# Kernel optimization log

Measured on AMD Instinct MI355X. Metric: run time of the kernel, lower is better.

Reference implementation:

```python
import jax, jax.numpy as jnp
import numpy as np
import math

B, S, D, H, DQ, DV, DI, L, V = 8, 512, 1024, 16, 64, 64, 4096, 6, 32000
EPS = 1e-5


def sinusoidal_pe(s, d):
    pos = np.arange(s)[:, None].astype(np.float64)
    i = np.arange(d)[None, :]
    angle = pos / np.power(10000.0, (2 * (i // 2)) / d)
    pe = np.where(i % 2 == 0, np.sin(angle), np.cos(angle))
    return jnp.asarray(pe, dtype=jnp.float32)  # [S, D]


def setup_inputs() -> dict:
    key = jax.random.key(0)
    ks = jax.random.split(key, 12)
    std = 0.02
    return {
        "tokens": jax.random.randint(ks[0], (B, S), 0, V),
        "lengths": jax.random.randint(ks[1], (B,), S // 2 + 1, S + 1),
        "emb": jax.random.normal(ks[2], (V, D), jnp.float32) * std,
        "Wq": jax.random.normal(ks[3], (L, D, H * DQ), jnp.float32) * std,
        "bq": jnp.zeros((L, H * DQ), jnp.float32),
        "Wkv": jax.random.normal(ks[4], (L, D, H * (DQ + DV)), jnp.float32) * std,
        "bkv": jnp.zeros((L, H * (DQ + DV)), jnp.float32),
        "Wo": jax.random.normal(ks[5], (L, H * DV, D), jnp.float32) * std,
        "bo": jnp.zeros((L, D), jnp.float32),
        "ln_attn_g": jnp.ones((L, D), jnp.float32),
        "ln_attn_b": jnp.zeros((L, D), jnp.float32),
        "W1": jax.random.normal(ks[6], (L, D, DI), jnp.float32) * std,
        "b1": jnp.zeros((L, DI), jnp.float32),
        "W2": jax.random.normal(ks[7], (L, DI, D), jnp.float32) * std,
        "b2": jnp.zeros((L, D), jnp.float32),
        "ln_ffn_g": jnp.ones((L, D), jnp.float32),
        "ln_ffn_b": jnp.zeros((L, D), jnp.float32),
        "ln_f_g": jnp.ones((D,), jnp.float32),
        "ln_f_b": jnp.zeros((D,), jnp.float32),
    }


def layer_norm(x, g, b):
    m = jnp.mean(x, axis=-1, keepdims=True)
    v = jnp.var(x, axis=-1, keepdims=True)
    return (x - m) / jnp.sqrt(v + EPS) * g + b


def encoder_forward(tokens, lengths, emb, Wq, bq, Wkv, bkv, Wo, bo,
                    ln_attn_g, ln_attn_b, W1, b1, W2, b2,
                    ln_ffn_g, ln_ffn_b, ln_f_g, ln_f_b):
    x = emb[tokens] * math.sqrt(D) + sinusoidal_pe(S, D)[None]  # [B,S,D]
    key_mask = jnp.arange(S)[None, :] < lengths[:, None]        # [B,S] valid keys
    scale = 1.0 / math.sqrt(DQ)

    def layer(x, p):
        wq, bq_, wkv, bkv_, wo, bo_, g1, be1, w1, bf1, w2, bf2, g2, be2 = p
        # --- multi-head self-attention sublayer (pre-LN, residual from raw x) ---
        h = layer_norm(x, g1, be1)
        q = (h @ wq + bq_).reshape(B, S, H, DQ)
        kv = h @ wkv + bkv_
        k = kv[..., : H * DQ].reshape(B, S, H, DQ)
        v = kv[..., H * DQ:].reshape(B, S, H, DV)
        scores = jnp.einsum('bqhd,bkhd->bhqk', q, k) * scale
        scores = jnp.where(key_mask[:, None, None, :], scores, -jnp.inf)
        a = jax.nn.softmax(scores, axis=-1)
        o = jnp.einsum('bhqk,bkhd->bqhd', a, v).reshape(B, S, H * DV)
        x = x + o @ wo + bo_
        # --- position-wise FFN sublayer (pre-LN, residual) ---
        h2 = layer_norm(x, g2, be2)
        x = x + jax.nn.relu(h2 @ w1 + bf1) @ w2 + bf2
        return x, None

    x, _ = jax.lax.scan(layer, x, (Wq, bq, Wkv, bkv, Wo, bo,
                                   ln_attn_g, ln_attn_b, W1, b1, W2, b2,
                                   ln_ffn_g, ln_ffn_b))
    return layer_norm(x, ln_f_g, ln_f_b)


def reference(tokens, lengths, emb, Wq, bq, Wkv, bkv, Wo, bo,
              ln_attn_g, ln_attn_b, W1, b1, W2, b2,
              ln_ffn_g, ln_ffn_b, ln_f_g, ln_f_b):
    return encoder_forward(tokens, lengths, emb, Wq, bq, Wkv, bkv, Wo, bo,
                           ln_attn_g, ln_attn_b, W1, b1, W2, b2,
                           ln_ffn_g, ln_ffn_b, ln_f_g, ln_f_b)
```

## Files before the change

kernel.cpp:

```cpp
#include <hip/hip_runtime.h>
#include <hip/hip_bf16.h>
#include <math.h>

typedef __bf16 bf16;
typedef bf16 bf16x8 __attribute__((ext_vector_type(8)));
typedef bf16 bf16x4v __attribute__((ext_vector_type(4)));
typedef float f32x4 __attribute__((ext_vector_type(4)));

typedef const __attribute__((address_space(1))) void* gp_t;
typedef __attribute__((address_space(3))) void* lp_t;

#define SB 512
#define DM 1024

__global__ __launch_bounds__(256) void embed_kernel(
    const int* __restrict__ tokens, const float* __restrict__ emb,
    float* __restrict__ x)
{
  const int row = blockIdx.x;
  const int s = row & (SB - 1);
  const int tok = tokens[row];
  const int c = threadIdx.x * 4;
  const float4 e = *(const float4*)&emb[(size_t)tok * DM + c];
  const float ev[4] = {e.x, e.y, e.z, e.w};
  float o[4];
#pragma unroll
  for (int u = 0; u < 4; ++u) {
    int i = c + u;
    int j = i & ~1;
    float freq = __expf(-9.210340371976184f * (float)j * (1.0f / (float)DM));
    float ang = (float)s * freq;
    float pe = ((i & 1) == 0) ? __sinf(ang) : __cosf(ang);
    o[u] = ev[u] * 32.0f + pe;
  }
  *(float4*)&x[(size_t)row * DM + c] = make_float4(o[0], o[1], o[2], o[3]);
}

template<bool OUTBF>
__global__ __launch_bounds__(256) void ln_kernel(
    const float* __restrict__ x, const float* __restrict__ g,
    const float* __restrict__ b, bf16* __restrict__ outB,
    float* __restrict__ outF)
{
  __shared__ float red[8];
  const int row = blockIdx.x, tid = threadIdx.x;
  const float4 v = *(const float4*)&x[(size_t)row * DM + tid * 4];
  float s = v.x + v.y + v.z + v.w;
  float sq = v.x * v.x + v.y * v.y + v.z * v.z + v.w * v.w;
#pragma unroll
  for (int off = 32; off > 0; off >>= 1) {
    s  += __shfl_xor(s, off);
    sq += __shfl_xor(sq, off);
  }
  if ((tid & 63) == 0) { red[tid >> 6] = s; red[4 + (tid >> 6)] = sq; }
  __syncthreads();
  const float ts = red[0] + red[1] + red[2] + red[3];
  const float tq = red[4] + red[5] + red[6] + red[7];
  const float mean = ts * (1.0f / DM);
  const float var  = tq * (1.0f / DM) - mean * mean;
  const float rstd = rsqrtf(var + 1e-5f);
  const int c = tid * 4;
  const float4 gv = *(const float4*)&g[c];
  const float4 bv = *(const float4*)&b[c];
  const float o0 = (v.x - mean) * rstd * gv.x + bv.x;
  const float o1 = (v.y - mean) * rstd * gv.y + bv.y;
  const float o2 = (v.z - mean) * rstd * gv.z + bv.z;
  const float o3 = (v.w - mean) * rstd * gv.w + bv.w;
  if constexpr (OUTBF) {
    bf16x4v ov = {(bf16)o0, (bf16)o1, (bf16)o2, (bf16)o3};
    *(bf16x4v*)&outB[(size_t)row * DM + c] = ov;
  } else {
    *(float4*)&outF[(size_t)row * DM + c] = make_float4(o0, o1, o2, o3);
  }
}

template<int NS, bool OUTBF, bool WRITEX>
__global__ __launch_bounds__(256) void red_ln_kernel(
    const float* __restrict__ x, const float* __restrict__ part,
    const float* __restrict__ badd, const float* __restrict__ g,
    const float* __restrict__ b, float* __restrict__ xout,
    bf16* __restrict__ outB, float* __restrict__ outF)
{
  __shared__ float red[8];
  const int row = blockIdx.x, tid = threadIdx.x;
  const int c = tid * 4;
  const size_t base = (size_t)row * DM + c;
  float4 v = *(const float4*)&x[base];
  const float4 ba = *(const float4*)&badd[c];
  v.x += ba.x; v.y += ba.y; v.z += ba.z; v.w += ba.w;
#pragma unroll
  for (int z = 0; z < NS; ++z) {
    const float4 pv = *(const float4*)&part[(size_t)z * 4096 * DM + base];
    v.x += pv.x; v.y += pv.y; v.z += pv.z; v.w += pv.w;
  }
  if constexpr (WRITEX) *(float4*)&xout[base] = v;
  float s = v.x + v.y + v.z + v.w;
  float sq = v.x * v.x + v.y * v.y + v.z * v.z + v.w * v.w;
#pragma unroll
  for (int off = 32; off > 0; off >>= 1) {
    s  += __shfl_xor(s, off);
    sq += __shfl_xor(sq, off);
  }
  if ((tid & 63) == 0) { red[tid >> 6] = s; red[4 + (tid >> 6)] = sq; }
  __syncthreads();
  const float ts = red[0] + red[1] + red[2] + red[3];
  const float tq = red[4] + red[5] + red[6] + red[7];
  const float mean = ts * (1.0f / DM);
  const float var  = tq * (1.0f / DM) - mean * mean;
  const float rstd = rsqrtf(var + 1e-5f);
  const float4 gv = *(const float4*)&g[c];
  const float4 bv = *(const float4*)&b[c];
  const float o0 = (v.x - mean) * rstd * gv.x + bv.x;
  const float o1 = (v.y - mean) * rstd * gv.y + bv.y;
  const float o2 = (v.z - mean) * rstd * gv.z + bv.z;
  const float o3 = (v.w - mean) * rstd * gv.w + bv.w;
  if constexpr (OUTBF) {
    bf16x4v ov = {(bf16)o0, (bf16)o1, (bf16)o2, (bf16)o3};
    *(bf16x4v*)&outB[(size_t)row * DM + c] = ov;
  } else {
    *(float4*)&outF[(size_t)row * DM + c] = make_float4(o0, o1, o2, o3);
  }
}

__global__ __launch_bounds__(256) void wtrans_kernel(
    const float* __restrict__ W, bf16* __restrict__ Wt, int N, int K)
{
  __shared__ __attribute__((aligned(16))) bf16 T[64][72];
  const int tid = threadIdx.x;
  const int n0 = blockIdx.x * 64;
  const int k0 = blockIdx.y * 64;
#pragma unroll
  for (int p = 0; p < 4; ++p) {
    const int flat = p * 1024 + tid * 4;
    const int kr = flat >> 6;
    const int nc = flat & 63;
    const float4 v = *(const float4*)&W[(size_t)(k0 + kr) * N + n0 + nc];
    T[nc + 0][kr] = (bf16)v.x;
    T[nc + 1][kr] = (bf16)v.y;
    T[nc + 2][kr] = (bf16)v.z;
    T[nc + 3][kr] = (bf16)v.w;
  }
  __syncthreads();
#pragma unroll
  for (int p = 0; p < 2; ++p) {
    const int flat = p * 2048 + tid * 8;
    const int nr = flat >> 6;
    const int kc = flat & 63;
    const bf16x8 v = *(const bf16x8*)&T[nr][kc];
    *(bf16x8*)&Wt[(size_t)(n0 + nr) * K + k0 + kc] = v;
  }
}

__global__ __launch_bounds__(256) void bias_concat_kernel(
    const float* __restrict__ bq, const float* __restrict__ bkv,
    float* __restrict__ bqkv)
{
  const int i = blockIdx.x * 256 + threadIdx.x;
  const int l = i / 3072, j = i - l * 3072;
  bqkv[i] = (j < 1024) ? bq[l * 1024 + j] : bkv[l * 2048 + (j - 1024)];
}

template<bool RELU, bool RESID, bool OUTBF, bool SPLITK>
__global__ __launch_bounds__(256) void gemm128(
    const bf16* __restrict__ A, const bf16* __restrict__ Bt,
    const float* __restrict__ bias, const float* __restrict__ resid,
    bf16* __restrict__ outB, float* __restrict__ outF,
    int M, int N, int K)
{
  __shared__ __attribute__((aligned(16))) bf16 As[128][32];
  __shared__ __attribute__((aligned(16))) bf16 Bs[128][32];
  const int tid  = threadIdx.x;
  const int lane = tid & 63;
  const int w    = tid >> 6;
  const int quad = lane >> 4;
  const int l16  = lane & 15;
  const int wr = w >> 1, wc = w & 1;

  const int gx    = gridDim.x;
  const int nwg   = gx * gridDim.y;
  const int orig  = blockIdx.y * gx + blockIdx.x;
  const int chunk = nwg >> 3;
  const int nl    = (orig & 7) * chunk + (orig >> 3);
  const int m0 = (nl / gx) * 128;
  const int n0 = (nl % gx) * 128;

  const int kspan = K / (int)gridDim.z;
  const int kbeg  = blockIdx.z * kspan;

  f32x4 acc[4][4] = {};

  const int r0 = tid >> 2;
  const int kg = (tid & 3) << 3;
  const bf16* a0 = &A [(size_t)(m0 + r0)      * K + kg];
  const bf16* a1 = &A [(size_t)(m0 + 64 + r0) * K + kg];
  const bf16* b0 = &Bt[(size_t)(n0 + r0)      * K + kg];
  const bf16* b1 = &Bt[(size_t)(n0 + 64 + r0) * K + kg];
  bf16* asd0 = &As[0][0] + (size_t)tid * 8;
  bf16* asd1 = &As[0][0] + (size_t)(256 + tid) * 8;
  bf16* bsd0 = &Bs[0][0] + (size_t)tid * 8;
  bf16* bsd1 = &Bs[0][0] + (size_t)(256 + tid) * 8;

  for (int k0 = kbeg; k0 < kbeg + kspan; k0 += 32) {
    __syncthreads();
    __builtin_amdgcn_global_load_lds((gp_t)(a0 + k0), (lp_t)asd0, 16, 0, 0);
    __builtin_amdgcn_global_load_lds((gp_t)(a1 + k0), (lp_t)asd1, 16, 0, 0);
    __builtin_amdgcn_global_load_lds((gp_t)(b0 + k0), (lp_t)bsd0, 16, 0, 0);
    __builtin_amdgcn_global_load_lds((gp_t)(b1 + k0), (lp_t)bsd1, 16, 0, 0);
    __syncthreads();

    bf16x8 af[4], bfg[4];
#pragma unroll
    for (int mt = 0; mt < 4; ++mt)
      af[mt] = *(const bf16x8*)&As[(wr << 6) + (mt << 4) + l16][quad << 3];
#pragma unroll
    for (int nt = 0; nt < 4; ++nt)
      bfg[nt] = *(const bf16x8*)&Bs[(wc << 6) + (nt << 4) + l16][quad << 3];
#pragma unroll
    for (int mt = 0; mt < 4; ++mt)
#pragma unroll
      for (int nt = 0; nt < 4; ++nt)
        acc[mt][nt] = __builtin_amdgcn_mfma_f32_16x16x32_bf16(af[mt], bfg[nt], acc[mt][nt], 0, 0, 0);
  }

  const int rbase = quad << 2;
  const size_t zoff = (size_t)blockIdx.z * M * N;
#pragma unroll
  for (int nt = 0; nt < 4; ++nt) {
    const int col = n0 + (wc << 6) + (nt << 4) + l16;
    const float bb = SPLITK ? 0.0f : bias[col];
#pragma unroll
    for (int mt = 0; mt < 4; ++mt) {
#pragma unroll
      for (int r = 0; r < 4; ++r) {
        const int row = m0 + (wr << 6) + (mt << 4) + rbase + r;
        float val = acc[mt][nt][r] + bb;
        if constexpr (SPLITK) {
          outF[zoff + (size_t)row * N + col] = val;
        } else {
          if constexpr (RESID) val += resid[(size_t)row * N + col];
          if constexpr (RELU)  val = fmaxf(val, 0.f);
          if constexpr (OUTBF) outB[(size_t)row * N + col] = (bf16)val;
          else                 outF[(size_t)row * N + col] = val;
        }
      }
    }
  }
}

__global__ __launch_bounds__(256) void attn_kernel(
    const bf16* __restrict__ qkv, const int* __restrict__ lengths,
    bf16* __restrict__ o)
{
  __shared__ __attribute__((aligned(16))) bf16 Qs[64][64];
  __shared__ __attribute__((aligned(16))) bf16 Ks[64][64];
  __shared__ __attribute__((aligned(16))) bf16 Vs[64][64];
  __shared__ __attribute__((aligned(16))) bf16 Vt[64][64];
  __shared__ __attribute__((aligned(16))) bf16 Ps[4][16][64];

  const int tid  = threadIdx.x;
  const int lane = tid & 63;
  const int w    = tid >> 6;
  const int quad = lane >> 4;
  const int l16  = lane & 15;
  const int qt = blockIdx.x, hh = blockIdx.y, b = blockIdx.z;
  const int q0 = qt * 64;
  const int len = lengths[b];
  const float scale = 0.125f;

#pragma unroll
  for (int r = 0; r < 2; ++r) {
    const int slot = tid + 256 * r;
    const int row = slot >> 3, dg = (slot & 7) << 3;
    *(bf16x8*)&Qs[row][dg ^ ((row & 7) << 3)] =
        *(const bf16x8*)&qkv[(size_t)(b * SB + q0 + row) * 3072 + hh * 64 + dg];
  }

  f32x4 Oacc[4] = {};
  float m_i[4] = {-1e30f, -1e30f, -1e30f, -1e30f};
  float l_i[4] = {0.f, 0.f, 0.f, 0.f};

  for (int kt0 = 0; kt0 < SB; kt0 += 64) {
    if (kt0 >= len) break;
    __syncthreads();
#pragma unroll
    for (int r = 0; r < 2; ++r) {
      const int slot = tid + 256 * r;
      const int row = slot >> 3, dg = (slot & 7) << 3;
      const size_t gbase = (size_t)(b * SB + kt0 + row) * 3072 + hh * 64 + dg;
      *(bf16x8*)&Ks[row][dg ^ ((row & 7) << 3)] =
          *(const bf16x8*)&qkv[gbase + 1024];
      *(bf16x8*)&Vs[row][dg] =
          *(const bf16x8*)&qkv[gbase + 2048];
    }
    __syncthreads();

    f32x4 s[4] = {};
    const int qrow = (w << 4) + l16;
#pragma unroll
    for (int ds = 0; ds < 2; ++ds) {
      const int cbase = (ds << 5) + (quad << 3);
      const bf16x8 af = *(const bf16x8*)&Qs[qrow][cbase ^ ((qrow & 7) << 3)];
#pragma unroll
      for (int nt = 0; nt < 4; ++nt) {
        const int krow = (nt << 4) + l16;
        const bf16x8 bfr = *(const bf16x8*)&Ks[krow][cbase ^ ((krow & 7) << 3)];
        s[nt] = __builtin_amdgcn_mfma_f32_16x16x32_bf16(af, bfr, s[nt], 0, 0, 0);
      }
    }
#pragma unroll
    for (int nt = 0; nt < 4; ++nt) {
      const bool valid = (kt0 + (nt << 4) + l16) < len;
#pragma unroll
      for (int r = 0; r < 4; ++r)
        s[nt][r] = valid ? s[nt][r] * scale : -1e30f;
    }
    float mt[4];
#pragma unroll
    for (int r = 0; r < 4; ++r)
      mt[r] = fmaxf(fmaxf(s[0][r], s[1][r]), fmaxf(s[2][r], s[3][r]));
#pragma unroll
    for (int off = 1; off < 16; off <<= 1)
#pragma unroll
      for (int r = 0; r < 4; ++r)
        mt[r] = fmaxf(mt[r], __shfl_xor(mt[r], off));
    float alpha[4];
#pragma unroll
    for (int r = 0; r < 4; ++r) {
      const float mn = fmaxf(m_i[r], mt[r]);
      alpha[r] = __expf(m_i[r] - mn);
      m_i[r] = mn;
    }
    float rs[4] = {0.f, 0.f, 0.f, 0.f};
#pragma unroll
    for (int nt = 0; nt < 4; ++nt)
#pragma unroll
      for (int r = 0; r < 4; ++r) {
        const float pe = __expf(s[nt][r] - m_i[r]);
        s[nt][r] = pe;
        rs[r] += pe;
      }
#pragma unroll
    for (int off = 1; off < 16; off <<= 1)
#pragma unroll
      for (int r = 0; r < 4; ++r)
        rs[r] += __shfl_xor(rs[r], off);
#pragma unroll
    for (int r = 0; r < 4; ++r) l_i[r] = l_i[r] * alpha[r] + rs[r];
#pragma unroll
    for (int nt = 0; nt < 4; ++nt)
#pragma unroll
      for (int r = 0; r < 4; ++r) {
        const int prow = (quad << 2) + r;
        Ps[w][prow][((nt << 4) + l16) ^ ((prow & 7) << 3)] = (bf16)s[nt][r];
        Oacc[nt][r] *= alpha[r];
      }
#pragma unroll
    for (int r2 = 0; r2 < 2; ++r2) {
      const int dv = tid & 63;
      const int kg2 = ((tid >> 6) << 3) + (r2 << 5);
      bf16x8 vv;
#pragma unroll
      for (int u = 0; u < 8; ++u)
        vv[u] = Vs[kg2 + u][dv];
      *(bf16x8*)&Vt[dv][kg2 ^ ((dv & 7) << 3)] = vv;
    }
    __syncthreads();
#pragma unroll
    for (int ks = 0; ks < 2; ++ks) {
      const int cbase = (ks << 5) + (quad << 3);
      const bf16x8 af = *(const bf16x8*)&Ps[w][l16][cbase ^ ((l16 & 7) << 3)];
#pragma unroll
      for (int nt = 0; nt < 4; ++nt) {
        const int vrow = (nt << 4) + l16;
        const bf16x8 bfr = *(const bf16x8*)&Vt[vrow][cbase ^ ((vrow & 7) << 3)];
        Oacc[nt] = __builtin_amdgcn_mfma_f32_16x16x32_bf16(af, bfr, Oacc[nt], 0, 0, 0);
      }
    }
  }
  float inv[4];
#pragma unroll
  for (int r = 0; r < 4; ++r) inv[r] = 1.0f / l_i[r];
#pragma unroll
  for (int nt = 0; nt < 4; ++nt)
#pragma unroll
    for (int r = 0; r < 4; ++r) {
      const int row = b * SB + q0 + (w << 4) + (quad << 2) + r;
      const int col = hh * 64 + (nt << 4) + l16;
      o[(size_t)row * 1024 + col] = (bf16)(Oacc[nt][r] * inv[r]);
    }
}

extern "C" void kernel_launch(void* const* d_in, const int* in_sizes, int n_in,
                              void* d_out, int out_size, void* d_ws, size_t ws_size,
                              hipStream_t stream) {
  const int*   tokens = (const int*)  d_in[0];
  const int*   lengths= (const int*)  d_in[1];
  const float* emb    = (const float*)d_in[2];
  const float* Wq     = (const float*)d_in[3];
  const float* bq     = (const float*)d_in[4];
  const float* Wkv    = (const float*)d_in[5];
  const float* bkv    = (const float*)d_in[6];
  const float* Wo     = (const float*)d_in[7];
  const float* bo     = (const float*)d_in[8];
  const float* lag    = (const float*)d_in[9];
  const float* lab    = (const float*)d_in[10];
  const float* W1     = (const float*)d_in[11];
  const float* b1     = (const float*)d_in[12];
  const float* W2     = (const float*)d_in[13];
  const float* b2     = (const float*)d_in[14];
  const float* lfg    = (const float*)d_in[15];
  const float* lfb    = (const float*)d_in[16];
  const float* lgf    = (const float*)d_in[17];
  const float* lbf    = (const float*)d_in[18];

  char* p = (char*)d_ws;
  float* x     = (float*)p; p += (size_t)4096 * 1024 * 4;
  bf16*  h     = (bf16*)p;  p += (size_t)4096 * 1024 * 2;
  bf16*  qkv   = (bf16*)p;  p += (size_t)4096 * 3072 * 2;
  bf16*  o     = (bf16*)p;  p += (size_t)4096 * 1024 * 2;
  bf16*  mid   = (bf16*)p;  p += (size_t)4096 * 4096 * 2;
  bf16*  wqkvt = (bf16*)p;  p += (size_t)3072 * 1024 * 2;
  bf16*  wot   = (bf16*)p;  p += (size_t)1024 * 1024 * 2;
  bf16*  w1t   = (bf16*)p;  p += (size_t)4096 * 1024 * 2;
  bf16*  w2t   = (bf16*)p;  p += (size_t)1024 * 4096 * 2;
  float* bqkv  = (float*)p; p += (size_t)6 * 3072 * 4;
  p = (char*)(((size_t)p + 255) & ~(size_t)255);
  float* part  = (float*)p; p += (size_t)4 * 4096 * 1024 * 4;

  bias_concat_kernel<<<72, 256, 0, stream>>>(bq, bkv, bqkv);
  embed_kernel<<<4096, 256, 0, stream>>>(tokens, emb, x);

  for (int l = 0; l < 6; ++l) {
    wtrans_kernel<<<dim3(16, 16), 256, 0, stream>>>(
        Wq + (size_t)l * 1024 * 1024, wqkvt, 1024, 1024);
    wtrans_kernel<<<dim3(32, 16), 256, 0, stream>>>(
        Wkv + (size_t)l * 1024 * 2048, wqkvt + (size_t)1024 * 1024, 2048, 1024);
    wtrans_kernel<<<dim3(16, 16), 256, 0, stream>>>(
        Wo + (size_t)l * 1024 * 1024, wot, 1024, 1024);
    wtrans_kernel<<<dim3(64, 16), 256, 0, stream>>>(
        W1 + (size_t)l * 1024 * 4096, w1t, 4096, 1024);
    wtrans_kernel<<<dim3(16, 64), 256, 0, stream>>>(
        W2 + (size_t)l * 4096 * 1024, w2t, 1024, 4096);

    if (l == 0) {
      ln_kernel<true><<<4096, 256, 0, stream>>>(
          x, lag, lab, h, nullptr);
    } else {
      red_ln_kernel<4, true, true><<<4096, 256, 0, stream>>>(
          x, part, b2 + (size_t)(l - 1) * 1024,
          lag + (size_t)l * 1024, lab + (size_t)l * 1024, x, h, nullptr);
    }
    gemm128<false, false, true, false><<<dim3(24, 32), 256, 0, stream>>>(
        h, wqkvt, bqkv + (size_t)l * 3072, nullptr, qkv, nullptr, 4096, 3072, 1024);
    attn_kernel<<<dim3(8, 16, 8), 256, 0, stream>>>(qkv, lengths, o);
    gemm128<false, false, false, true><<<dim3(8, 32, 2), 256, 0, stream>>>(
        o, wot, nullptr, nullptr, nullptr, part, 4096, 1024, 1024);
    red_ln_kernel<2, true, true><<<4096, 256, 0, stream>>>(
        x, part, bo + (size_t)l * 1024,
        lfg + (size_t)l * 1024, lfb + (size_t)l * 1024, x, h, nullptr);
    gemm128<true, false, true, false><<<dim3(32, 32), 256, 0, stream>>>(
        h, w1t, b1 + (size_t)l * 4096, nullptr, mid, nullptr, 4096, 4096, 1024);
    gemm128<false, false, false, true><<<dim3(8, 32, 4), 256, 0, stream>>>(
        mid, w2t, nullptr, nullptr, nullptr, part, 4096, 1024, 4096);
  }
  red_ln_kernel<4, false, false><<<4096, 256, 0, stream>>>(
      x, part, b2 + (size_t)5 * 1024, lgf, lbf, nullptr, nullptr, (float*)d_out);
}
```

Baseline: 1.893 ms.

## Replace 128x128 GEMM with double-buffered 256x256 tile kernel with swizzled LDS

New measurement: 1.607 ms. 15.1% less time.

```diff
diff --git a/kernel.cpp b/kernel.cpp
--- a/kernel.cpp
+++ b/kernel.cpp
@@ -160,91 +160,125 @@
   bqkv[i] = (j < 1024) ? bq[l * 1024 + j] : bkv[l * 2048 + (j - 1024)];
 }
 
-template<bool RELU, bool RESID, bool OUTBF, bool SPLITK>
-__global__ __launch_bounds__(256) void gemm128(
+template<bool RELU, bool OUTBF, bool SPLITK>
+__global__ __launch_bounds__(512, 2) void gemm256(
     const bf16* __restrict__ A, const bf16* __restrict__ Bt,
-    const float* __restrict__ bias, const float* __restrict__ resid,
+    const float* __restrict__ bias,
     bf16* __restrict__ outB, float* __restrict__ outF,
     int M, int N, int K)
 {
-  __shared__ __attribute__((aligned(16))) bf16 As[128][32];
-  __shared__ __attribute__((aligned(16))) bf16 Bs[128][32];
+  __shared__ __attribute__((aligned(16))) bf16 sm[2][2][256 * 64];
+
   const int tid  = threadIdx.x;
   const int lane = tid & 63;
   const int w    = tid >> 6;
   const int quad = lane >> 4;
   const int l16  = lane & 15;
-  const int wr = w >> 1, wc = w & 1;
+  const int wm   = w >> 2;
+  const int wn   = w & 3;
 
   const int gx    = gridDim.x;
   const int nwg   = gx * gridDim.y;
   const int orig  = blockIdx.y * gx + blockIdx.x;
   const int chunk = nwg >> 3;
   const int nl    = (orig & 7) * chunk + (orig >> 3);
-  const int m0 = (nl / gx) * 128;
-  const int n0 = (nl % gx) * 128;
+  const int m0 = (nl / gx) * 256;
+  const int n0 = (nl % gx) * 256;
 
   const int kspan = K / (int)gridDim.z;
   const int kbeg  = blockIdx.z * kspan;
-
-  f32x4 acc[4][4] = {};
-
-  const int r0 = tid >> 2;
-  const int kg = (tid & 3) << 3;
-  const bf16* a0 = &A [(size_t)(m0 + r0)      * K + kg];
-  const bf16* a1 = &A [(size_t)(m0 + 64 + r0) * K + kg];
-  const bf16* b0 = &Bt[(size_t)(n0 + r0)      * K + kg];
-  const bf16* b1 = &Bt[(size_t)(n0 + 64 + r0) * K + kg];
-  bf16* asd0 = &As[0][0] + (size_t)tid * 8;
-  bf16* asd1 = &As[0][0] + (size_t)(256 + tid) * 8;
-  bf16* bsd0 = &Bs[0][0] + (size_t)tid * 8;
-  bf16* bsd1 = &Bs[0][0] + (size_t)(256 + tid) * 8;
-
-  for (int k0 = kbeg; k0 < kbeg + kspan; k0 += 32) {
+  const int ntile = kspan >> 6;
+
+  const int rowst = tid >> 3;
+  const int slot  = (tid & 7) ^ (rowst & 7);
+  const int colst = slot << 3;
+  const bf16* aSrc = A  + (size_t)(m0 + rowst) * K + kbeg + colst;
+  const bf16* bSrc = Bt + (size_t)(n0 + rowst) * K + kbeg + colst;
+
+  f32x4 acc[8][4] = {};
+  const int xm = (l16 & 7) << 3;
+
+#define STAGE256(buf, koff) do {                                           \
+    const bf16* as_ = aSrc + (koff);                                       \
+    const bf16* bs_ = bSrc + (koff);                                       \
+    bf16* ad_ = &sm[buf][0][tid * 8];                                      \
+    bf16* bd_ = &sm[buf][1][tid * 8];                                      \
+    _Pragma("unroll")                                                      \
+    for (int i_ = 0; i_ < 4; ++i_) {                                       \
+      __builtin_amdgcn_global_load_lds((gp_t)(as_ + (size_t)i_ * 64 * K),  \
+                                       (lp_t)(ad_ + i_ * 4096), 16, 0, 0); \
+      __builtin_amdgcn_global_load_lds((gp_t)(bs_ + (size_t)i_ * 64 * K),  \
+                                       (lp_t)(bd_ + i_ * 4096), 16, 0, 0); \
+    }                                                                      \
+  } while (0)
+
+  STAGE256(0, 0);
+  __syncthreads();
+
+  int cur = 0;
+  for (int t = 0; t < ntile; ++t) {
+    if (t + 1 < ntile) STAGE256(cur ^ 1, (t + 1) << 6);
+
+    const bf16* Ab = &sm[cur][0][0];
+    const bf16* Bb = &sm[cur][1][0];
+
+    bf16x8 bF[4][2];
+#pragma unroll
+    for (int nt = 0; nt < 4; ++nt)
+#pragma unroll
+      for (int ks = 0; ks < 2; ++ks) {
+        const int rowb = (wn << 6) + (nt << 4) + l16;
+        bF[nt][ks] = *(const bf16x8*)&Bb[rowb * 64 + (((ks << 5) + (quad << 3)) ^ xm)];
+      }
+#pragma unroll
+    for (int p = 0; p < 4; ++p) {
+      bf16x8 aF[2][2];
+#pragma unroll
+      for (int m2 = 0; m2 < 2; ++m2)
+#pragma unroll
+        for (int ks = 0; ks < 2; ++ks) {
+          const int rowa = (wm << 7) + (((p << 1) + m2) << 4) + l16;
+          aF[m2][ks] = *(const bf16x8*)&Ab[rowa * 64 + (((ks << 5) + (quad << 3)) ^ xm)];
+        }
+      __builtin_amdgcn_s_setprio(1);
+#pragma unroll
+      for (int m2 = 0; m2 < 2; ++m2)
+#pragma unroll
+        for (int nt = 0; nt < 4; ++nt)
+#pragma unroll
+          for (int ks = 0; ks < 2; ++ks)
+            acc[(p << 1) + m2][nt] = __builtin_amdgcn_mfma_f32_16x16x32_bf16(
+                aF[m2][ks], bF[nt][ks], acc[(p << 1) + m2][nt], 0, 0, 0);
+      __builtin_amdgcn_s_setprio(0);
+    }
     __syncthreads();
-    __builtin_amdgcn_global_load_lds((gp_t)(a0 + k0), (lp_t)asd0, 16, 0, 0);
-    __builtin_amdgcn_global_load_lds((gp_t)(a1 + k0), (lp_t)asd1, 16, 0, 0);
-    __builtin_amdgcn_global_load_lds((gp_t)(b0 + k0), (lp_t)bsd0, 16, 0, 0);
-    __builtin_amdgcn_global_load_lds((gp_t)(b1 + k0), (lp_t)bsd1, 16, 0, 0);
-    __syncthreads();
-
-    bf16x8 af[4], bfg[4];
-#pragma unroll
-    for (int mt = 0; mt < 4; ++mt)
-      af[mt] = *(const bf16x8*)&As[(wr << 6) + (mt << 4) + l16][quad << 3];
-#pragma unroll
-    for (int nt = 0; nt < 4; ++nt)
-      bfg[nt] = *(const bf16x8*)&Bs[(wc << 6) + (nt << 4) + l16][quad << 3];
-#pragma unroll
-    for (int mt = 0; mt < 4; ++mt)
-#pragma unroll
-      for (int nt = 0; nt < 4; ++nt)
-        acc[mt][nt] = __builtin_amdgcn_mfma_f32_16x16x32_bf16(af[mt], bfg[nt], acc[mt][nt], 0, 0, 0);
-  }
-
-  const int rbase = quad << 2;
-  const size_t zoff = (size_t)blockIdx.z * M * N;
-#pragma unroll
-  for (int nt = 0; nt < 4; ++nt) {
-    const int col = n0 + (wc << 6) + (nt << 4) + l16;
-    const float bb = SPLITK ? 0.0f : bias[col];
-#pragma unroll
-    for (int mt = 0; mt < 4; ++mt) {
-#pragma unroll
-      for (int r = 0; r < 4; ++r) {
-        const int row = m0 + (wr << 6) + (mt << 4) + rbase + r;
-        float val = acc[mt][nt][r] + bb;
-        if constexpr (SPLITK) {
-          outF[zoff + (size_t)row * N + col] = val;
-        } else {
-          if constexpr (RESID) val += resid[(size_t)row * N + col];
-          if constexpr (RELU)  val = fmaxf(val, 0.f);
-          if constexpr (OUTBF) outB[(size_t)row * N + col] = (bf16)val;
-          else                 outF[(size_t)row * N + col] = val;
+    cur ^= 1;
+  }
+
+  const int rb = quad << 2;
+#pragma unroll
+  for (int mt = 0; mt < 8; ++mt) {
+#pragma unroll
+    for (int nt = 0; nt < 4; ++nt) {
+      const int col  = n0 + (wn << 6) + (nt << 4) + l16;
+      const int rowg = m0 + (wm << 7) + (mt << 4) + rb;
+      if constexpr (SPLITK) {
+        float* dst = outF + (size_t)blockIdx.z * M * N + (size_t)rowg * N + col;
+#pragma unroll
+        for (int r = 0; r < 4; ++r) dst[(size_t)r * N] = acc[mt][nt][r];
+      } else {
+        const float bb = bias[col];
+#pragma unroll
+        for (int r = 0; r < 4; ++r) {
+          float v = acc[mt][nt][r] + bb;
+          if constexpr (RELU) v = fmaxf(v, 0.f);
+          if constexpr (OUTBF) outB[(size_t)(rowg + r) * N + col] = (bf16)v;
+          else                 outF[(size_t)(rowg + r) * N + col] = v;
         }
       }
     }
   }
+#undef STAGE256
 }
 
 __global__ __launch_bounds__(256) void attn_kernel(
@@ -450,18 +484,18 @@
           x, part, b2 + (size_t)(l - 1) * 1024,
           lag + (size_t)l * 1024, lab + (size_t)l * 1024, x, h, nullptr);
     }
-    gemm128<false, false, true, false><<<dim3(24, 32), 256, 0, stream>>>(
-        h, wqkvt, bqkv + (size_t)l * 3072, nullptr, qkv, nullptr, 4096, 3072, 1024);
+    gemm256<false, true, false><<<dim3(12, 16), 512, 0, stream>>>(
+        h, wqkvt, bqkv + (size_t)l * 3072, qkv, nullptr, 4096, 3072, 1024);
     attn_kernel<<<dim3(8, 16, 8), 256, 0, stream>>>(qkv, lengths, o);
-    gemm128<false, false, false, true><<<dim3(8, 32, 2), 256, 0, stream>>>(
-        o, wot, nullptr, nullptr, nullptr, part, 4096, 1024, 1024);
-    red_ln_kernel<2, true, true><<<4096, 256, 0, stream>>>(
+    gemm256<false, false, true><<<dim3(4, 16, 4), 512, 0, stream>>>(
+        o, wot, nullptr, nullptr, part, 4096, 1024, 1024);
+    red_ln_kernel<4, true, true><<<4096, 256, 0, stream>>>(
         x, part, bo + (size_t)l * 1024,
         lfg + (size_t)l * 1024, lfb + (size_t)l * 1024, x, h, nullptr);
-    gemm128<true, false, true, false><<<dim3(32, 32), 256, 0, stream>>>(
-        h, w1t, b1 + (size_t)l * 4096, nullptr, mid, nullptr, 4096, 4096, 1024);
-    gemm128<false, false, false, true><<<dim3(8, 32, 4), 256, 0, stream>>>(
-        mid, w2t, nullptr, nullptr, nullptr, part, 4096, 1024, 4096);
+    gemm256<true, true, false><<<dim3(16, 16), 512, 0, stream>>>(
+        h, w1t, b1 + (size_t)l * 4096, mid, nullptr, 4096, 4096, 1024);
+    gemm256<false, false, true><<<dim3(4, 16, 4), 512, 0, stream>>>(
+        mid, w2t, nullptr, nullptr, part, 4096, 1024, 4096);
   }
   red_ln_kernel<4, false, false><<<4096, 256, 0, stream>>>(
       x, part, b2 + (size_t)5 * 1024, lgf, lbf, nullptr, nullptr, (float*)d_out);
```
